# Kernel tuning notes

Hardware: AMD Instinct MI355X
Metric: run time of the kernel (lower is better)

The kernel has to match this reference:

```python
import jax, jax.numpy as jnp
import numpy as np

B, S, D, H, DK, DFF = 4, 1024, 1024, 16, 64, 4096
EPS = 1e-5


def layer_norm(x, g, b):
    m = jnp.mean(x, axis=-1, keepdims=True)
    v = jnp.var(x, axis=-1, keepdims=True)
    return (x - m) * jax.lax.rsqrt(v + EPS) * g + b


def setup_inputs() -> dict:
    key = jax.random.key(0)
    ks = jax.random.split(key, 12)
    sc = 0.02
    return {
        "x":    jax.random.normal(ks[0], (B, S, D), jnp.float32),
        # per-head Q/K/V projections, stacked over heads: [H, D, DK]
        "Wq":   jax.random.normal(ks[1], (H, D, DK), jnp.float32) * sc,
        "bq":   jnp.zeros((H, DK), jnp.float32),
        "Wk":   jax.random.normal(ks[2], (H, D, DK), jnp.float32) * sc,
        "bk":   jnp.zeros((H, DK), jnp.float32),
        "Wv":   jax.random.normal(ks[3], (H, D, DK), jnp.float32) * sc,
        "bv":   jnp.zeros((H, DK), jnp.float32),
        # output projection: [H*DK, D]
        "Wo":   jax.random.normal(ks[4], (H * DK, D), jnp.float32) * sc,
        "bo":   jnp.zeros((D,), jnp.float32),
        # FFN
        "W1":   jax.random.normal(ks[5], (D, DFF), jnp.float32) * sc,
        "b1":   jnp.zeros((DFF,), jnp.float32),
        "W2":   jax.random.normal(ks[6], (DFF, D), jnp.float32) * sc,
        "b2":   jnp.zeros((D,), jnp.float32),
        # LayerNorms
        "g1":   jnp.ones((D,), jnp.float32),
        "be1":  jnp.zeros((D,), jnp.float32),
        "g2":   jnp.ones((D,), jnp.float32),
        "be2":  jnp.zeros((D,), jnp.float32),
    }


def reference(x, Wq, bq, Wk, bk, Wv, bv, Wo, bo, W1, b1, W2, b2, g1, be1, g2, be2):
    # batched multi-head attention (original loops per head; math identical)
    q = jnp.einsum("bsd,hdk->bhsk", x, Wq) + bq[None, :, None, :]
    k = jnp.einsum("bsd,hdk->bhsk", x, Wk) + bk[None, :, None, :]
    v = jnp.einsum("bsd,hdk->bhsk", x, Wv) + bv[None, :, None, :]
    scale = 1.0 / jnp.sqrt(jnp.asarray(DK, x.dtype))
    scores = jnp.einsum("bhsk,bhtk->bhst", q * scale, k)
    attn = jax.nn.softmax(scores, axis=-1)  # dropout = eval-mode identity
    o = jnp.einsum("bhst,bhtk->bhsk", attn, v)
    # torch.cat over heads along dim 2 -> [B, S, H*DK]
    o = jnp.transpose(o, (0, 2, 1, 3)).reshape(B, S, H * DK)
    att = o @ Wo + bo
    # post-attn: residual of LayerNorm(att)
    x = x + layer_norm(att, g1, be1)
    # FFN
    pos = jax.nn.relu(x @ W1 + b1) @ W2 + b2
    x = x + layer_norm(pos, g2, be2)
    return x
```

## Files before the change

### kernel.cpp

```cpp
#include <hip/hip_runtime.h>
#include <hip/hip_bf16.h>
#include <hip/hip_fp16.h>

typedef unsigned short u16;
typedef short bf16x8_t __attribute__((ext_vector_type(8)));
typedef float f32x4_t  __attribute__((ext_vector_type(4)));

__device__ __forceinline__ u16 f2bf(float f) {
    __hip_bfloat16 h = __float2bfloat16(f);
    union { __hip_bfloat16 b; u16 u; } cv; cv.b = h; return cv.u;
}

__device__ __forceinline__ void g2l16(const void* g, void* l) {
    __builtin_amdgcn_global_load_lds(
        (const __attribute__((address_space(1))) unsigned int*)g,
        (__attribute__((address_space(3))) unsigned int*)l, 16, 0, 0);
}

__global__ __launch_bounds__(256)
void k_prep(const float* __restrict__ x, u16* __restrict__ Xb,
            const float* __restrict__ Wq, const float* __restrict__ Wk,
            const float* __restrict__ Wv, u16* __restrict__ Wqkvt,
            const float* __restrict__ Wo, const float* __restrict__ W1,
            const float* __restrict__ W2, u16* __restrict__ Wot,
            u16* __restrict__ W1t, u16* __restrict__ W2t)
{
    int id = blockIdx.x;
    if (id < 4096) {
        int i = id * 256 + threadIdx.x;
        float4 f = ((const float4*)x)[i];
        ushort4 o;
        o.x = f2bf(f.x); o.y = f2bf(f.y); o.z = f2bf(f.z); o.w = f2bf(f.w);
        ((ushort4*)Xb)[i] = o;
        return;
    }
    id -= 4096;
    const float* in; u16* out; int R, C, r0, c0;
    if (id < 768) {
        int zx = id >> 8, hy = (id >> 4) & 15, tx = id & 15;
        in  = (zx == 0 ? Wq : (zx == 1 ? Wk : Wv)) + (size_t)hy * 65536;
        out = Wqkvt + ((size_t)zx * 1024 + hy * 64) * 1024;
        R = 1024; C = 64; r0 = tx * 64; c0 = 0;
    } else {
        id -= 768;
        int tx, ty;
        if (id < 256)       { in = Wo; out = Wot; R = 1024; C = 1024; tx = id & 15; ty = id >> 4; }
        else if (id < 1280) { id -= 256; in = W1; out = W1t; R = 1024; C = 4096; tx = id & 63; ty = id >> 6; }
        else                { id -= 1280; in = W2; out = W2t; R = 4096; C = 1024; tx = id & 15; ty = id >> 4; }
        r0 = ty * 64; c0 = tx * 64;
    }
    __shared__ float t[64][65];
    int lc = threadIdx.x & 63, lr = threadIdx.x >> 6;
#pragma unroll
    for (int p = 0; p < 16; ++p) {
        int rr = p * 4 + lr;
        t[rr][lc] = in[(size_t)(r0 + rr) * C + c0 + lc];
    }
    __syncthreads();
#pragma unroll
    for (int p = 0; p < 16; ++p) {
        int cc = p * 4 + lr;
        out[(size_t)(c0 + cc) * R + r0 + lc] = f2bf(t[lc][cc]);
    }
}

__global__ __launch_bounds__(256)
void k_vt(const u16* __restrict__ V, u16* __restrict__ VT) {
    __shared__ u16 t[64 * 72];
    int bh = blockIdx.y, s0 = blockIdx.x * 64;
    const u16* Vp = V + (size_t)bh * 65536;
    u16* Tp = VT + (size_t)bh * 65536;
    int tid = threadIdx.x;
    int r = tid >> 3, c = (tid & 7) * 8;
    *(uint4*)&t[r * 72 + c]        = *(const uint4*)&Vp[(size_t)(s0 + r) * 64 + c];
    *(uint4*)&t[(r + 32) * 72 + c] = *(const uint4*)&Vp[(size_t)(s0 + r + 32) * 64 + c];
    __syncthreads();
    int d = tid >> 2, sl0 = (tid & 3) * 16;
    uint4 outv[2];
    u16* ov = (u16*)outv;
#pragma unroll
    for (int j = 0; j < 16; ++j) ov[j] = t[(sl0 + j) * 72 + d];
    *(uint4*)&Tp[(size_t)d * 1024 + s0 + sl0]     = outv[0];
    *(uint4*)&Tp[(size_t)d * 1024 + s0 + sl0 + 8] = outv[1];
}

__global__ __launch_bounds__(256, 4)
void k_gemm_bt(const u16* __restrict__ A, const u16* __restrict__ Bt,
               void* __restrict__ out, int M, int N, int K, int kchunk)
{
    __shared__ __align__(16) u16 As[2 * 128 * 32];
    __shared__ __align__(16) u16 Bs[2 * 128 * 32];
    int tid = threadIdx.x;
    int wave = tid >> 6, lane = tid & 63;

    int nx = gridDim.x, nwg = nx * gridDim.y;
    int f  = blockIdx.x + nx * blockIdx.y;
    int f2 = (f & 7) * (nwg >> 3) + (f >> 3);
    int bx = f2 % nx, by = f2 / nx;
    int row0 = by * 128, col0 = bx * 128;

    int z = blockIdx.z;
    int kbeg = z * kchunk;

    int lrow = lane >> 2, lcol = (lane & 3) * 8;
    const u16* pA0 = A  + (size_t)(row0 + wave * 16 + lrow) * K + kbeg + lcol;
    const u16* pA1 = pA0 + (size_t)64 * K;
    const u16* pB0 = Bt + (size_t)(col0 + wave * 16 + lrow) * K + kbeg + lcol;
    const u16* pB1 = pB0 + (size_t)64 * K;
    u16* lA0 = &As[wave * 512];
    u16* lA1 = &As[2048 + wave * 512];
    u16* lB0 = &Bs[wave * 512];
    u16* lB1 = &Bs[2048 + wave * 512];

    int wm = (wave >> 1) * 64, wn = (wave & 1) * 64;
    int quad = lane >> 4, l16 = lane & 15;

    f32x4_t acc[4][4];
#pragma unroll
    for (int i = 0; i < 4; i++)
#pragma unroll
        for (int j = 0; j < 4; j++) acc[i][j] = f32x4_t{0.f, 0.f, 0.f, 0.f};

    for (int kk = 0; kk < kchunk; kk += 64) {
        __syncthreads();
        g2l16(pA0, lA0);      g2l16(pA1, lA1);
        g2l16(pA0 + 32, lA0 + 4096); g2l16(pA1 + 32, lA1 + 4096);
        g2l16(pB0, lB0);      g2l16(pB1, lB1);
        g2l16(pB0 + 32, lB0 + 4096); g2l16(pB1 + 32, lB1 + 4096);
        pA0 += 64; pA1 += 64; pB0 += 64; pB1 += 64;
        __syncthreads();

#pragma unroll
        for (int s = 0; s < 2; ++s) {
            const u16* as = &As[s * 4096];
            const u16* bs = &Bs[s * 4096];
            bf16x8_t a[4], b[4];
#pragma unroll
            for (int i = 0; i < 4; ++i)
                a[i] = *(const bf16x8_t*)&as[(wm + i * 16 + l16) * 32 + quad * 8];
#pragma unroll
            for (int j = 0; j < 4; ++j)
                b[j] = *(const bf16x8_t*)&bs[(wn + j * 16 + l16) * 32 + quad * 8];
#pragma unroll
            for (int i = 0; i < 4; ++i)
#pragma unroll
                for (int j = 0; j < 4; ++j)
                    acc[i][j] = __builtin_amdgcn_mfma_f32_16x16x32_bf16(a[i], b[j], acc[i][j], 0, 0, 0);
        }
    }

#pragma unroll
    for (int i = 0; i < 4; ++i)
#pragma unroll
        for (int j = 0; j < 4; ++j)
#pragma unroll
            for (int r = 0; r < 4; ++r) {
                int row = row0 + wm + i * 16 + quad * 4 + r;
                int col = col0 + wn + j * 16 + l16;
                ((__half*)out)[(size_t)z * M * N + (size_t)row * N + col] =
                    __float2half(acc[i][j][r]);
            }
}

template<int EPI>
__device__ __forceinline__
void gemm256x128(const u16* __restrict__ A, const u16* __restrict__ Bt,
                 const float* __restrict__ bias0, const float* __restrict__ bias1,
                 const float* __restrict__ bias2, void* __restrict__ out,
                 int M, int N, int K, int kchunk, int z, int bx, int by)
{
    __shared__ __align__(16) u16 As[2 * 256 * 32];
    __shared__ __align__(16) u16 Bs[2 * 128 * 32];
    int tid = threadIdx.x;
    int wave = tid >> 6, lane = tid & 63;
    int row0 = by * 256, col0 = bx * 128;
    int kbeg = z * kchunk;

    int lrow = lane >> 2, lcol = (lane & 3) * 8;
    const u16* pA0 = A  + (size_t)(row0 + wave * 16 + lrow) * K + kbeg + lcol;
    const u16* pA1 = pA0 + (size_t)128 * K;
    const u16* pB0 = Bt + (size_t)(col0 + wave * 16 + lrow) * K + kbeg + lcol;
    u16* lA0 = &As[wave * 512];
    u16* lA1 = &As[4096 + wave * 512];
    u16* lB0 = &Bs[wave * 512];

    int wm = (wave >> 1) * 64, wn = (wave & 1) * 64;
    int quad = lane >> 4, l16 = lane & 15;

    f32x4_t acc[4][4];
#pragma unroll
    for (int i = 0; i < 4; i++)
#pragma unroll
        for (int j = 0; j < 4; j++) acc[i][j] = f32x4_t{0.f, 0.f, 0.f, 0.f};

    for (int kk = 0; kk < kchunk; kk += 64) {
        __syncthreads();
        g2l16(pA0, lA0);           g2l16(pA1, lA1);
        g2l16(pA0 + 32, lA0 + 8192); g2l16(pA1 + 32, lA1 + 8192);
        g2l16(pB0, lB0);           g2l16(pB0 + 32, lB0 + 4096);
        pA0 += 64; pA1 += 64; pB0 += 64;
        __syncthreads();

#pragma unroll
        for (int s = 0; s < 2; ++s) {
            const u16* as = &As[s * 8192];
            const u16* bs = &Bs[s * 4096];
            bf16x8_t a[4], b[4];
#pragma unroll
            for (int i = 0; i < 4; ++i)
                a[i] = *(const bf16x8_t*)&as[(wm + i * 16 + l16) * 32 + quad * 8];
#pragma unroll
            for (int j = 0; j < 4; ++j)
                b[j] = *(const bf16x8_t*)&bs[(wn + j * 16 + l16) * 32 + quad * 8];
#pragma unroll
            for (int i = 0; i < 4; ++i)
#pragma unroll
                for (int j = 0; j < 4; ++j)
                    acc[i][j] = __builtin_amdgcn_mfma_f32_16x16x32_bf16(a[i], b[j], acc[i][j], 0, 0, 0);
        }
    }

#pragma unroll
    for (int i = 0; i < 4; ++i)
#pragma unroll
        for (int j = 0; j < 4; ++j)
#pragma unroll
            for (int r = 0; r < 4; ++r) {
                int row = row0 + wm + i * 16 + quad * 4 + r;
                int col = col0 + wn + j * 16 + l16;
                float v = acc[i][j][r];
                if (EPI == 0) {
                    ((__half*)out)[(size_t)z * M * N + (size_t)row * N + col] = __float2half(v);
                } else if (EPI == 1) {
                    ((u16*)out)[(size_t)row * N + col] = f2bf(fmaxf(v + bias0[col], 0.f));
                } else {
                    int proj = col >> 10, within = col & 1023;
                    const float* bp = proj == 0 ? bias0 : (proj == 1 ? bias1 : bias2);
                    v += bp[within];
                    if (proj == 0) v *= 0.18033688f;
                    int h = within >> 6, kq = within & 63;
                    int b_ = row >> 10, s_ = row & 1023;
                    size_t bh = (size_t)((b_ << 4) + h);
                    ((u16*)out)[(size_t)proj * 4194304 + bh * 65536 + (s_ << 6) + kq] = f2bf(v);
                }
            }
}

__global__ __launch_bounds__(512, 4)
void k_gemm_qkv(const u16* __restrict__ A, const u16* __restrict__ Bt,
                const float* __restrict__ bq, const float* __restrict__ bk,
                const float* __restrict__ bv, void* __restrict__ out,
                int M, int N, int K)
{
    gemm256x128<2>(A, Bt, bq, bk, bv, out, M, N, K, K, 0, blockIdx.x, blockIdx.y);
}

__global__ __launch_bounds__(512, 4)
void k_gemm_ffn1(const u16* __restrict__ A, const u16* __restrict__ Bt,
                 const float* __restrict__ b1, void* __restrict__ out,
                 int M, int N, int K)
{
    gemm256x128<1>(A, Bt, b1, nullptr, nullptr, out, M, N, K, K, 0, blockIdx.x, blockIdx.y);
}

__global__ __launch_bounds__(512, 4)
void k_gemm_ffn2(const u16* __restrict__ A, const u16* __restrict__ Bt,
                 void* __restrict__ out, int M, int N, int K, int kchunk)
{
    int nx = gridDim.x, nwg = nx * gridDim.y;
    int f  = blockIdx.x + nx * blockIdx.y;
    int f2 = (f & 7) * (nwg >> 3) + (f >> 3);
    gemm256x128<0>(A, Bt, nullptr, nullptr, nullptr, out, M, N, K, kchunk,
                   blockIdx.z, f2 % nx, f2 / nx);
}

__global__ __launch_bounds__(512, 4)
void k_attn(const u16* __restrict__ Qg, const u16* __restrict__ Kg,
            const u16* __restrict__ VTg, u16* __restrict__ Og)
{
    __shared__ __align__(16) u16 Ks[64 * 64];
    __shared__ __align__(16) u16 Vs[64 * 64];
    __shared__ __align__(16) u16 Ps[128 * 64];

    int tid = threadIdx.x, wave = tid >> 6, lane = tid & 63;
    int quad = lane >> 4, l16 = lane & 15;

    int f  = blockIdx.x + gridDim.x * blockIdx.y;
    int f2 = (f & 7) * ((gridDim.x * gridDim.y) >> 3) + (f >> 3);
    int bh = f2 >> 3;
    int q0 = (f2 & 7) * 128;
    int wrow = wave * 16;

    const u16* Qp  = Qg  + (size_t)bh * 65536;
    const u16* Kp  = Kg  + (size_t)bh * 65536;
    const u16* VTp = VTg + (size_t)bh * 65536;

    int arow_g = q0 + wrow + l16;
    bf16x8_t aq0 = *(const bf16x8_t*)&Qp[(size_t)arow_g * 64 + quad * 8];
    bf16x8_t aq1 = *(const bf16x8_t*)&Qp[(size_t)arow_g * 64 + 32 + quad * 8];

    int srow = tid >> 3, scb = tid & 7;
    uint4 kreg = *(const uint4*)&Kp[(size_t)srow * 64 + scb * 8];
    uint4 vreg = *(const uint4*)&VTp[(size_t)srow * 1024 + scb * 8];
    u16* kdst = &Ks[srow * 64 + ((scb ^ (srow & 7)) * 8)];
    u16* vdst = &Vs[srow * 64 + ((scb ^ (srow & 7)) * 8)];

    f32x4_t o[4], lsum;
#pragma unroll
    for (int nt = 0; nt < 4; ++nt) o[nt] = f32x4_t{0.f, 0.f, 0.f, 0.f};
    lsum = f32x4_t{0.f, 0.f, 0.f, 0.f};

    bf16x8_t ones;
#pragma unroll
    for (int j = 0; j < 8; ++j) ones[j] = (short)0x3F80;

    int a7 = l16 & 7;

    for (int kv0 = 0; kv0 < 1024; kv0 += 64) {
        __syncthreads();
        *(uint4*)kdst = kreg;
        *(uint4*)vdst = vreg;
        __syncthreads();
        if (kv0 < 960) {
            kreg = *(const uint4*)&Kp[(size_t)(kv0 + 64 + srow) * 64 + scb * 8];
            vreg = *(const uint4*)&VTp[(size_t)srow * 1024 + kv0 + 64 + scb * 8];
        }

        f32x4_t s[4];
#pragma unroll
        for (int nt = 0; nt < 4; ++nt) {
            int brow = nt * 16 + l16;
            bf16x8_t bk0 = *(const bf16x8_t*)&Ks[brow * 64 + ((quad ^ a7) * 8)];
            bf16x8_t bk1 = *(const bf16x8_t*)&Ks[brow * 64 + (((4 + quad) ^ a7) * 8)];
            s[nt] = __builtin_amdgcn_mfma_f32_16x16x32_bf16(aq0, bk0, f32x4_t{0.f,0.f,0.f,0.f}, 0, 0, 0);
            s[nt] = __builtin_amdgcn_mfma_f32_16x16x32_bf16(aq1, bk1, s[nt], 0, 0, 0);
        }

#pragma unroll
        for (int nt = 0; nt < 4; ++nt) {
            int pcb = nt * 2 + (l16 >> 3);
#pragma unroll
            for (int r = 0; r < 4; ++r) {
                float p = exp2f(s[nt][r]);
                int pr = wrow + quad * 4 + r;
                Ps[pr * 64 + ((pcb ^ (pr & 7)) * 8) + (l16 & 7)] = f2bf(p);
            }
        }

        int arow = wrow + l16;
        bf16x8_t ap0 = *(const bf16x8_t*)&Ps[arow * 64 + ((quad ^ a7) * 8)];
        bf16x8_t ap1 = *(const bf16x8_t*)&Ps[arow * 64 + (((4 + quad) ^ a7) * 8)];
#pragma unroll
        for (int nt = 0; nt < 4; ++nt) {
            int vrow = nt * 16 + l16;
            bf16x8_t bv0 = *(const bf16x8_t*)&Vs[vrow * 64 + ((quad ^ a7) * 8)];
            bf16x8_t bv1 = *(const bf16x8_t*)&Vs[vrow * 64 + (((4 + quad) ^ a7) * 8)];
            o[nt] = __builtin_amdgcn_mfma_f32_16x16x32_bf16(ap0, bv0, o[nt], 0, 0, 0);
            o[nt] = __builtin_amdgcn_mfma_f32_16x16x32_bf16(ap1, bv1, o[nt], 0, 0, 0);
        }
        lsum = __builtin_amdgcn_mfma_f32_16x16x32_bf16(ap0, ones, lsum, 0, 0, 0);
        lsum = __builtin_amdgcn_mfma_f32_16x16x32_bf16(ap1, ones, lsum, 0, 0, 0);
    }

    int b = bh >> 4, h = bh & 15;
    float invl[4];
#pragma unroll
    for (int r = 0; r < 4; ++r) invl[r] = 1.f / lsum[r];
#pragma unroll
    for (int nt = 0; nt < 4; ++nt)
#pragma unroll
        for (int r = 0; r < 4; ++r) {
            int srow2 = q0 + wrow + quad * 4 + r;
            Og[(size_t)(b * 1024 + srow2) * 1024 + (h << 6) + nt * 16 + l16] = f2bf(o[nt][r] * invl[r]);
        }
}

template<int MODE, int NP>
__global__ __launch_bounds__(256)
void k_ln2(const __half* __restrict__ p, const float* __restrict__ bias,
           const float* __restrict__ residf, const u16* __restrict__ residb,
           const float* __restrict__ g, const float* __restrict__ be,
           float* __restrict__ out, u16* __restrict__ outb)
{
    int row = blockIdx.x, tid = threadIdx.x;
    size_t base = (size_t)row * 1024;
    float xv[4]; float s = 0.f, sq = 0.f;
#pragma unroll
    for (int i = 0; i < 4; i++) {
        int c = tid + i * 256;
        float t = bias[c];
#pragma unroll
        for (int z = 0; z < NP; ++z) t += __half2float(p[(size_t)z * 4194304 + base + c]);
        xv[i] = t;
        s += t; sq += t * t;
    }
#pragma unroll
    for (int off = 32; off; off >>= 1) { s += __shfl_down(s, off); sq += __shfl_down(sq, off); }
    __shared__ float ss[4], ssq[4];
    int wv = tid >> 6;
    if ((tid & 63) == 0) { ss[wv] = s; ssq[wv] = sq; }
    __syncthreads();
    s  = ss[0] + ss[1] + ss[2] + ss[3];
    sq = ssq[0] + ssq[1] + ssq[2] + ssq[3];
    float mean = s * (1.f / 1024.f);
    float var  = sq * (1.f / 1024.f) - mean * mean;
    float rstd = rsqrtf(var + 1e-5f);
#pragma unroll
    for (int i = 0; i < 4; i++) {
        int c = tid + i * 256;
        float rv;
        if (MODE == 0) rv = residf[base + c];
        else {
            union { u16 u[2]; unsigned int w; float f; } cv;
            cv.w = (unsigned int)residb[base + c] << 16;
            rv = cv.f;
        }
        float y = rv + (xv[i] - mean) * rstd * g[c] + be[c];
        if (MODE == 0) outb[base + c] = f2bf(y);
        else           out[base + c] = y;
    }
}

extern "C" void kernel_launch(void* const* d_in, const int* in_sizes, int n_in,
                              void* d_out, int out_size, void* d_ws, size_t ws_size,
                              hipStream_t stream) {
    const float* x   = (const float*)d_in[0];
    const float* Wq  = (const float*)d_in[1];
    const float* bq  = (const float*)d_in[2];
    const float* Wk  = (const float*)d_in[3];
    const float* bk  = (const float*)d_in[4];
    const float* Wv  = (const float*)d_in[5];
    const float* bv  = (const float*)d_in[6];
    const float* Wo  = (const float*)d_in[7];
    const float* bo  = (const float*)d_in[8];
    const float* W1  = (const float*)d_in[9];
    const float* b1  = (const float*)d_in[10];
    const float* W2  = (const float*)d_in[11];
    const float* b2  = (const float*)d_in[12];
    const float* g1  = (const float*)d_in[13];
    const float* be1 = (const float*)d_in[14];
    const float* g2  = (const float*)d_in[15];
    const float* be2 = (const float*)d_in[16];
    float* out = (float*)d_out;

    char* w = (char*)d_ws;
    u16*    Xb    = (u16*)(w);
    u16*    VTb   = (u16*)(w);
    u16*    Wqkvt = (u16*)(w + 8388608);
    u16*    Wot   = (u16*)(w + 14680064);
    u16*    W1t   = (u16*)(w + 16777216);
    u16*    W2t   = (u16*)(w + 25165824);
    u16*    Qb    = (u16*)(w + 33554432);
    u16*    Kb    = (u16*)(w + 41943040);
    u16*    Vb    = (u16*)(w + 50331648);
    u16*    Oc    = (u16*)(w + 58720256);
    __half* part4 = (__half*)(w + 33554432);
    __half* part2 = (__half*)(w + 67108864);
    u16*    x1b   = (u16*)(w + 117440512);
    u16*    hb    = (u16*)(w + 125829120);

    k_prep<<<7168, 256, 0, stream>>>(x, Xb, Wq, Wk, Wv, Wqkvt, Wo, W1, W2, Wot, W1t, W2t);

    k_gemm_qkv<<<dim3(24, 16), 512, 0, stream>>>(Xb, Wqkvt, bq, bk, bv, Qb, 4096, 3072, 1024);

    k_vt<<<dim3(16, 64), 256, 0, stream>>>(Vb, VTb);

    k_attn<<<dim3(8, 64), 512, 0, stream>>>(Qb, Kb, VTb, Oc);

    k_gemm_bt<<<dim3(8, 32, 2), 256, 0, stream>>>(Oc, Wot, part2, 4096, 1024, 1024, 512);

    k_ln2<0, 2><<<4096, 256, 0, stream>>>(part2, bo, x, nullptr, g1, be1, nullptr, x1b);

    k_gemm_ffn1<<<dim3(32, 16), 512, 0, stream>>>(x1b, W1t, b1, hb, 4096, 4096, 1024);

    k_gemm_ffn2<<<dim3(8, 16, 4), 512, 0, stream>>>(hb, W2t, part4, 4096, 1024, 4096, 1024);

    k_ln2<1, 4><<<4096, 256, 0, stream>>>(part4, b2, nullptr, x1b, g2, be2, out, nullptr);
}
```

Before: 311.7 us.

## Double-buffer attention K/V tiles, raise MFMA priority, vectorize LayerNorm loads

New measurement: 311.7 us. Within noise of the previous version (-0.0%).

```diff
diff --git a/kernel.cpp b/kernel.cpp
--- a/kernel.cpp
+++ b/kernel.cpp
@@ -9,6 +9,10 @@
 __device__ __forceinline__ u16 f2bf(float f) {
     __hip_bfloat16 h = __float2bfloat16(f);
     union { __hip_bfloat16 b; u16 u; } cv; cv.b = h; return cv.u;
+}
+
+__device__ __forceinline__ float bf2f(u16 u) {
+    union { unsigned int w; float f; } cv; cv.w = (unsigned int)u << 16; return cv.f;
 }
 
 __device__ __forceinline__ void g2l16(const void* g, void* l) {
@@ -278,8 +282,8 @@
 void k_attn(const u16* __restrict__ Qg, const u16* __restrict__ Kg,
             const u16* __restrict__ VTg, u16* __restrict__ Og)
 {
-    __shared__ __align__(16) u16 Ks[64 * 64];
-    __shared__ __align__(16) u16 Vs[64 * 64];
+    __shared__ __align__(16) u16 Ks[2][64 * 64];
+    __shared__ __align__(16) u16 Vs[2][64 * 64];
     __shared__ __align__(16) u16 Ps[128 * 64];
 
     int tid = threadIdx.x, wave = tid >> 6, lane = tid & 63;
@@ -300,10 +304,10 @@
     bf16x8_t aq1 = *(const bf16x8_t*)&Qp[(size_t)arow_g * 64 + 32 + quad * 8];
 
     int srow = tid >> 3, scb = tid & 7;
+    int sdoff = srow * 64 + ((scb ^ (srow & 7)) * 8);
+
     uint4 kreg = *(const uint4*)&Kp[(size_t)srow * 64 + scb * 8];
     uint4 vreg = *(const uint4*)&VTp[(size_t)srow * 1024 + scb * 8];
-    u16* kdst = &Ks[srow * 64 + ((scb ^ (srow & 7)) * 8)];
-    u16* vdst = &Vs[srow * 64 + ((scb ^ (srow & 7)) * 8)];
 
     f32x4_t o[4], lsum;
 #pragma unroll
@@ -316,25 +320,34 @@
 
     int a7 = l16 & 7;
 
-    for (int kv0 = 0; kv0 < 1024; kv0 += 64) {
-        __syncthreads();
-        *(uint4*)kdst = kreg;
-        *(uint4*)vdst = vreg;
-        __syncthreads();
-        if (kv0 < 960) {
-            kreg = *(const uint4*)&Kp[(size_t)(kv0 + 64 + srow) * 64 + scb * 8];
-            vreg = *(const uint4*)&VTp[(size_t)srow * 1024 + kv0 + 64 + scb * 8];
+    *(uint4*)&Ks[0][sdoff] = kreg;
+    *(uint4*)&Vs[0][sdoff] = vreg;
+    kreg = *(const uint4*)&Kp[(size_t)(64 + srow) * 64 + scb * 8];
+    vreg = *(const uint4*)&VTp[(size_t)srow * 1024 + 64 + scb * 8];
+    __syncthreads();
+
+    for (int t = 0; t < 16; ++t) {
+        int cur = t & 1, nxt = cur ^ 1;
+        if (t < 15) {
+            *(uint4*)&Ks[nxt][sdoff] = kreg;
+            *(uint4*)&Vs[nxt][sdoff] = vreg;
+        }
+        if (t < 14) {
+            kreg = *(const uint4*)&Kp[(size_t)((t + 2) * 64 + srow) * 64 + scb * 8];
+            vreg = *(const uint4*)&VTp[(size_t)srow * 1024 + (t + 2) * 64 + scb * 8];
         }
 
         f32x4_t s[4];
+        __builtin_amdgcn_s_setprio(1);
 #pragma unroll
         for (int nt = 0; nt < 4; ++nt) {
             int brow = nt * 16 + l16;
-            bf16x8_t bk0 = *(const bf16x8_t*)&Ks[brow * 64 + ((quad ^ a7) * 8)];
-            bf16x8_t bk1 = *(const bf16x8_t*)&Ks[brow * 64 + (((4 + quad) ^ a7) * 8)];
+            bf16x8_t bk0 = *(const bf16x8_t*)&Ks[cur][brow * 64 + ((quad ^ a7) * 8)];
+            bf16x8_t bk1 = *(const bf16x8_t*)&Ks[cur][brow * 64 + (((4 + quad) ^ a7) * 8)];
             s[nt] = __builtin_amdgcn_mfma_f32_16x16x32_bf16(aq0, bk0, f32x4_t{0.f,0.f,0.f,0.f}, 0, 0, 0);
             s[nt] = __builtin_amdgcn_mfma_f32_16x16x32_bf16(aq1, bk1, s[nt], 0, 0, 0);
         }
+        __builtin_amdgcn_s_setprio(0);
 
 #pragma unroll
         for (int nt = 0; nt < 4; ++nt) {
@@ -350,16 +363,19 @@
         int arow = wrow + l16;
         bf16x8_t ap0 = *(const bf16x8_t*)&Ps[arow * 64 + ((quad ^ a7) * 8)];
         bf16x8_t ap1 = *(const bf16x8_t*)&Ps[arow * 64 + (((4 + quad) ^ a7) * 8)];
+        __builtin_amdgcn_s_setprio(1);
 #pragma unroll
         for (int nt = 0; nt < 4; ++nt) {
             int vrow = nt * 16 + l16;
-            bf16x8_t bv0 = *(const bf16x8_t*)&Vs[vrow * 64 + ((quad ^ a7) * 8)];
-            bf16x8_t bv1 = *(const bf16x8_t*)&Vs[vrow * 64 + (((4 + quad) ^ a7) * 8)];
+            bf16x8_t bv0 = *(const bf16x8_t*)&Vs[cur][vrow * 64 + ((quad ^ a7) * 8)];
+            bf16x8_t bv1 = *(const bf16x8_t*)&Vs[cur][vrow * 64 + (((4 + quad) ^ a7) * 8)];
             o[nt] = __builtin_amdgcn_mfma_f32_16x16x32_bf16(ap0, bv0, o[nt], 0, 0, 0);
             o[nt] = __builtin_amdgcn_mfma_f32_16x16x32_bf16(ap1, bv1, o[nt], 0, 0, 0);
         }
         lsum = __builtin_amdgcn_mfma_f32_16x16x32_bf16(ap0, ones, lsum, 0, 0, 0);
         lsum = __builtin_amdgcn_mfma_f32_16x16x32_bf16(ap1, ones, lsum, 0, 0, 0);
+        __builtin_amdgcn_s_setprio(0);
+        __syncthreads();
     }
 
     int b = bh >> 4, h = bh & 15;
@@ -384,16 +400,22 @@
 {
     int row = blockIdx.x, tid = threadIdx.x;
     size_t base = (size_t)row * 1024;
-    float xv[4]; float s = 0.f, sq = 0.f;
-#pragma unroll
-    for (int i = 0; i < 4; i++) {
-        int c = tid + i * 256;
-        float t = bias[c];
-#pragma unroll
-        for (int z = 0; z < NP; ++z) t += __half2float(p[(size_t)z * 4194304 + base + c]);
-        xv[i] = t;
-        s += t; sq += t * t;
-    }
+    int c0 = tid * 4;
+    float xv[4];
+    {
+        float4 b4 = *(const float4*)&bias[c0];
+        xv[0] = b4.x; xv[1] = b4.y; xv[2] = b4.z; xv[3] = b4.w;
+    }
+#pragma unroll
+    for (int z = 0; z < NP; ++z) {
+        union { uint2 u; __half h[4]; } cv;
+        cv.u = *(const uint2*)&p[(size_t)z * 4194304 + base + c0];
+#pragma unroll
+        for (int i = 0; i < 4; ++i) xv[i] += __half2float(cv.h[i]);
+    }
+    float s = 0.f, sq = 0.f;
+#pragma unroll
+    for (int i = 0; i < 4; ++i) { s += xv[i]; sq += xv[i] * xv[i]; }
 #pragma unroll
     for (int off = 32; off; off >>= 1) { s += __shfl_down(s, off); sq += __shfl_down(sq, off); }
     __shared__ float ss[4], ssq[4];
@@ -405,19 +427,29 @@
     float mean = s * (1.f / 1024.f);
     float var  = sq * (1.f / 1024.f) - mean * mean;
     float rstd = rsqrtf(var + 1e-5f);
-#pragma unroll
-    for (int i = 0; i < 4; i++) {
-        int c = tid + i * 256;
-        float rv;
-        if (MODE == 0) rv = residf[base + c];
-        else {
-            union { u16 u[2]; unsigned int w; float f; } cv;
-            cv.w = (unsigned int)residb[base + c] << 16;
-            rv = cv.f;
-        }
-        float y = rv + (xv[i] - mean) * rstd * g[c] + be[c];
-        if (MODE == 0) outb[base + c] = f2bf(y);
-        else           out[base + c] = y;
+
+    float4 g4  = *(const float4*)&g[c0];
+    float4 be4 = *(const float4*)&be[c0];
+    float gv[4] = {g4.x, g4.y, g4.z, g4.w};
+    float bv[4] = {be4.x, be4.y, be4.z, be4.w};
+    float rv[4];
+    if (MODE == 0) {
+        float4 r4 = *(const float4*)&residf[base + c0];
+        rv[0] = r4.x; rv[1] = r4.y; rv[2] = r4.z; rv[3] = r4.w;
+    } else {
+        ushort4 rb = *(const ushort4*)&residb[base + c0];
+        rv[0] = bf2f(rb.x); rv[1] = bf2f(rb.y); rv[2] = bf2f(rb.z); rv[3] = bf2f(rb.w);
+    }
+    float y[4];
+#pragma unroll
+    for (int i = 0; i < 4; ++i) y[i] = rv[i] + (xv[i] - mean) * rstd * gv[i] + bv[i];
+    if (MODE == 0) {
+        ushort4 o;
+        o.x = f2bf(y[0]); o.y = f2bf(y[1]); o.z = f2bf(y[2]); o.w = f2bf(y[3]);
+        *(ushort4*)&outb[base + c0] = o;
+    } else {
+        float4 o; o.x = y[0]; o.y = y[1]; o.z = y[2]; o.w = y[3];
+        *(float4*)&out[base + c0] = o;
     }
 }
 
```
